# Performance work log

Hardware: AMD Instinct MI355X
Metric: run time of the kernel (lower is better)

Reference implementation:

```python
import jax, jax.numpy as jnp
import numpy as np
from jax import lax

# Module config (matches init_kwargs)
C_IN, C_OUT, D_STATE = 512, 256, 16
D_INNER = 2 * C_OUT          # canonical Mamba expand=2
DT_RANK = C_OUT // 16        # ceil(256/16) = 16
D_CONV = 4
BN_EPS = 1e-5


def setup_inputs() -> dict:
    key = jax.random.key(0)
    ks = jax.random.split(key, 16)
    s = 0.02
    B, H, W = 8, 64, 64
    inp = {
        "x": jax.random.normal(ks[0], (B, C_IN, H, W), jnp.float32),
        # lateral 1x1 conv
        "lateral_w": jax.random.normal(ks[1], (C_OUT, C_IN), jnp.float32) * s,
        "lateral_b": jnp.zeros((C_OUT,), jnp.float32),
        # mamba block params
        "in_proj_w": jax.random.normal(ks[2], (2 * D_INNER, C_OUT), jnp.float32) * s,
        "conv1d_w": jax.random.normal(ks[3], (D_INNER, D_CONV), jnp.float32) * s,
        "conv1d_b": jnp.zeros((D_INNER,), jnp.float32),
        "x_proj_w": jax.random.normal(ks[4], (DT_RANK + 2 * D_STATE, D_INNER), jnp.float32) * s,
        "dt_proj_w": jax.random.normal(ks[5], (D_INNER, DT_RANK), jnp.float32) * s,
        "dt_proj_b": jnp.full((D_INNER,), -4.0, jnp.float32),  # softplus -> small dt
        "A_log": jnp.log(jnp.broadcast_to(jnp.arange(1, D_STATE + 1, dtype=jnp.float32), (D_INNER, D_STATE))),  # S4D-real init
        "D_param": jnp.ones((D_INNER,), jnp.float32),
        "out_proj_w": jax.random.normal(ks[6], (C_OUT, D_INNER), jnp.float32) * s,
        # refine: 3x3 conv + BN (eval) + ReLU
        "refine_w": jax.random.normal(ks[7], (C_OUT, C_OUT, 3, 3), jnp.float32) * s,
        "refine_b": jnp.zeros((C_OUT,), jnp.float32),
        "bn_gamma": jnp.ones((C_OUT,), jnp.float32),
        "bn_beta": jnp.zeros((C_OUT,), jnp.float32),
        "bn_mean": jnp.zeros((C_OUT,), jnp.float32),
        "bn_var": jnp.ones((C_OUT,), jnp.float32),
    }
    return inp


def _silu(v):
    return v * jax.nn.sigmoid(v)


def _mamba(u, in_proj_w, conv1d_w, conv1d_b, x_proj_w, dt_proj_w, dt_proj_b,
           A_log, D_param, out_proj_w):
    """Canonical Mamba block on u: (B, L, D) -> (B, L, D)."""
    B, L, D = u.shape
    xz = jnp.einsum('bld,ed->ble', u, in_proj_w)            # (B,L,2*d_inner)
    xm, z = jnp.split(xz, 2, axis=-1)
    # causal depthwise conv1d over L
    xc = xm.transpose(0, 2, 1)                               # (B,d_inner,L)
    xc = lax.conv_general_dilated(xc, conv1d_w[:, None, :], (1,),
                                  [(D_CONV - 1, 0)],
                                  feature_group_count=D_INNER)
    xc = _silu(xc + conv1d_b[None, :, None]).transpose(0, 2, 1)  # (B,L,d_inner)
    proj = jnp.einsum('bld,ed->ble', xc, x_proj_w)           # (B,L,dt_rank+2*N)
    dt_r = proj[..., :DT_RANK]
    B_ssm = proj[..., DT_RANK:DT_RANK + D_STATE]             # (B,L,N)
    C_ssm = proj[..., DT_RANK + D_STATE:]                    # (B,L,N)
    dt = jax.nn.softplus(jnp.einsum('blr,dr->bld', dt_r, dt_proj_w) + dt_proj_b)
    A = -jnp.exp(A_log)                                      # (d_inner,N)

    def step(h, inputs):
        dt_t, B_t, C_t, x_t = inputs                         # (B,d), (B,N), (B,N), (B,d)
        dA = jnp.exp(dt_t[..., None] * A)                    # (B,d,N)
        h = dA * h + dt_t[..., None] * B_t[:, None, :] * x_t[..., None]
        y = jnp.einsum('bdn,bn->bd', h, C_t)
        return h, y

    xs = (dt.transpose(1, 0, 2), B_ssm.transpose(1, 0, 2),
          C_ssm.transpose(1, 0, 2), xc.transpose(1, 0, 2))
    h0 = jnp.zeros((B, D_INNER, D_STATE), u.dtype)
    _, ys = lax.scan(step, h0, xs)                           # (L,B,d_inner)
    y = ys.transpose(1, 0, 2) + xc * D_param
    y = y * _silu(z)
    return jnp.einsum('ble,de->bld', y, out_proj_w)          # (B,L,D)


def reference(x, lateral_w, lateral_b, in_proj_w, conv1d_w, conv1d_b, x_proj_w,
              dt_proj_w, dt_proj_b, A_log, D_param, out_proj_w, refine_w,
              refine_b, bn_gamma, bn_beta, bn_mean, bn_var):
    B, _, H, W = x.shape
    # lateral 1x1 conv
    xl = jnp.einsum('oi,bihw->bohw', lateral_w, x) + lateral_b[None, :, None, None]
    # mamba on flattened spatial sequence, residual add
    u = xl.reshape(B, C_OUT, H * W).transpose(0, 2, 1)        # (B,L,C)
    m = _mamba(u, in_proj_w, conv1d_w, conv1d_b, x_proj_w, dt_proj_w,
               dt_proj_b, A_log, D_param, out_proj_w)
    xr = xl + m.transpose(0, 2, 1).reshape(B, C_OUT, H, W)
    # refine: 3x3 conv + BN(eval) + ReLU
    r = lax.conv_general_dilated(xr, refine_w, (1, 1), [(1, 1), (1, 1)])
    r = r + refine_b[None, :, None, None]
    inv = bn_gamma / jnp.sqrt(bn_var + BN_EPS)
    r = (r - bn_mean[None, :, None, None]) * inv[None, :, None, None] + bn_beta[None, :, None, None]
    return jax.nn.relu(r)
```

## Files before the change

kernel.cpp:

```cpp
#include <hip/hip_runtime.h>
#include <math.h>

#define NB   8
#define CIN  512
#define COUT 256
#define DIN  512
#define LHW  4096
#define NCHK 256
#define CHL  16
#define PW   66
#define PPOS (PW*PW)

typedef __attribute__((ext_vector_type(8))) short bf16x8;
typedef __attribute__((ext_vector_type(4))) float f32x4;
typedef __attribute__((ext_vector_type(2))) float f32x2;

__device__ __forceinline__ float siluf(float v)  { return v / (1.f + __expf(-v)); }
__device__ __forceinline__ float splusf(float v) {
  return fmaxf(v, 0.f) + __logf(1.f + __expf(-fabsf(v)));
}

__device__ __forceinline__ unsigned short f2b(float f) {
  union { float f; unsigned u; } v; v.f = f;
  unsigned r = v.u + 0x7fff + ((v.u >> 16) & 1);
  return (unsigned short)(r >> 16);
}
__device__ __forceinline__ float b2f(unsigned int u) {
  union { unsigned u; float f; } v; v.u = (u & 0xffffu) << 16; return v.f;
}

__device__ __forceinline__ f32x2 pk_fma(f32x2 a, f32x2 b, f32x2 c) {
  f32x2 d;
  asm("v_pk_fma_f32 %0, %1, %2, %3" : "=v"(d) : "v"(a), "v"(b), "v"(c));
  return d;
}
__device__ __forceinline__ f32x2 pk_mul(f32x2 a, f32x2 b) {
  f32x2 d;
  asm("v_pk_mul_f32 %0, %1, %2" : "=v"(d) : "v"(a), "v"(b));
  return d;
}

__device__ __forceinline__ void gload16(const unsigned short* g, unsigned short* l) {
  __builtin_amdgcn_global_load_lds(
      (const __attribute__((address_space(1))) unsigned int*)g,
      (__attribute__((address_space(3))) unsigned int*)l, 16, 0, 0);
}

#define WO1 131072
#define WO2 393216
#define WO3 425984
#define WO4 557056
#define WO5 1146880
#define WO6 1474560
#define WPN 1482752
__global__ __launch_bounds__(256)
void k_wprep(const float* __restrict__ lw, const float* __restrict__ ipw,
             const float* __restrict__ xpw, const float* __restrict__ opw,
             const float* __restrict__ rw, const float* __restrict__ dtpw,
             const float* __restrict__ A_log,
             unsigned short* __restrict__ wb, unsigned short* __restrict__ wfb,
             float* __restrict__ Antab) {
  const int i = blockIdx.x * 256 + threadIdx.x;
  if (i < WO1)      wb[i] = f2b(lw[i]);
  else if (i < WO2) wb[i] = f2b(ipw[i - WO1]);
  else if (i < WO3) {
    const int j = i - WO2, row = j >> 9, col = j & 511;
    wb[i] = (row < 48) ? f2b(xpw[row * 512 + col]) : (unsigned short)0;
  }
  else if (i < WO4) wb[i] = f2b(opw[i - WO3]);
  else if (i < WO5) {
    const int j = i - WO4, o = j / 2304, kk = j % 2304;
    const int tap = kk >> 8, ch = kk & 255;
    wb[i] = f2b(rw[(o * 256 + ch) * 9 + tap]);
  }
  else if (i < WO6) {
    const int j = i - WO5, row = j >> 9, e = j & 511;
    float v = 0.f;
    if (row < 512) {
#pragma unroll
      for (int r = 0; r < 16; ++r)
        v = fmaf(dtpw[row * 16 + r], xpw[r * 512 + e], v);
    } else if (row < 560) {
      v = xpw[(row - 512) * 512 + e];
    }
    wfb[j] = f2b(v);
  }
  else if (i < WPN) {
    const int j = i - WO6;
    Antab[j] = -__expf(A_log[j]);
  }
}

__global__ __launch_bounds__(256)
void k_border(unsigned int* __restrict__ xrp_u) {
  const int i = blockIdx.x * 256 + threadIdx.x;
  if (i >= 8 * 260 * 128) return;
  const int b  = i / (260 * 128);
  const int r  = i - b * 260 * 128;
  const int p  = r >> 7;
  const int ci = r & 127;
  int y, x;
  if (p < 66)       { y = 0;       x = p; }
  else if (p < 132) { y = 65;      x = p - 66; }
  else if (p < 196) { x = 0;       y = p - 131; }
  else              { x = 65;      y = p - 195; }
  xrp_u[(((size_t)b * PPOS + y * PW + x) * COUT >> 1) + ci] = 0u;
}

__global__ __launch_bounds__(256)
void k_xpose(const float* __restrict__ x, unsigned short* __restrict__ xt) {
  __shared__ unsigned short Ts[64][80];
  const int b  = blockIdx.z;
  const int k0 = blockIdx.y * 64;
  const int l0 = blockIdx.x * 64;
  const int t  = threadIdx.x;
  const int tx = t & 15, ty = t >> 4;
#pragma unroll
  for (int r = 0; r < 4; ++r) {
    const int k = ty + r * 16;
    float4 v = *(const float4*)(x + ((size_t)b * CIN + k0 + k) * LHW + l0 + tx * 4);
    Ts[tx*4+0][k] = f2b(v.x);
    Ts[tx*4+1][k] = f2b(v.y);
    Ts[tx*4+2][k] = f2b(v.z);
    Ts[tx*4+3][k] = f2b(v.w);
  }
  __syncthreads();
  const int lr = t >> 2, kc = (t & 3) * 16;
  unsigned short* dst = xt + ((size_t)b * LHW + l0 + lr) * CIN + k0 + kc;
  *(uint4*)dst       = *(const uint4*)&Ts[lr][kc];
  *(uint4*)(dst + 8) = *(const uint4*)&Ts[lr][kc + 8];
}

template<int RSA, int RSB, int KTOT>
__device__ __forceinline__ void gemm_loop_128(
    const unsigned short* __restrict__ Ab, const unsigned short* __restrict__ Bb,
    unsigned short (&As)[2][4096], unsigned short (&Bs)[2][4096],
    int t, f32x4 acc[4][4]) {
  const int w = t >> 6, lane = t & 63;
  const int wm = w >> 1, wn = w & 1;
  const int arow = t >> 2;
  const int acol = (((t & 3) ^ ((t >> 3) & 3))) * 8;
  const int fr = lane & 15;
  const int g8 = ((lane >> 4) * 8) ^ (((fr >> 1) & 3) * 8);
  for (int k0 = 0; k0 < KTOT; k0 += 64) {
    __syncthreads();
    gload16(Ab + (size_t)arow * RSA + k0 + acol,             &As[0][w * 512]);
    gload16(Ab + (size_t)(64 + arow) * RSA + k0 + acol,      &As[0][2048 + w*512]);
    gload16(Bb + (size_t)arow * RSB + k0 + acol,             &Bs[0][w * 512]);
    gload16(Bb + (size_t)(64 + arow) * RSB + k0 + acol,      &Bs[0][2048 + w*512]);
    gload16(Ab + (size_t)arow * RSA + k0 + 32 + acol,        &As[1][w * 512]);
    gload16(Ab + (size_t)(64 + arow) * RSA + k0 + 32 + acol, &As[1][2048 + w*512]);
    gload16(Bb + (size_t)arow * RSB + k0 + 32 + acol,        &Bs[1][w * 512]);
    gload16(Bb + (size_t)(64 + arow) * RSB + k0 + 32 + acol, &Bs[1][2048 + w*512]);
    __syncthreads();
#pragma unroll
    for (int h = 0; h < 2; ++h) {
      bf16x8 af[4], bf[4];
#pragma unroll
      for (int f = 0; f < 4; ++f) {
        af[f] = *(const bf16x8*)&As[h][(wm*64 + f*16 + fr) * 32 + g8];
        bf[f] = *(const bf16x8*)&Bs[h][(wn*64 + f*16 + fr) * 32 + g8];
      }
#pragma unroll
      for (int i = 0; i < 4; ++i)
#pragma unroll
        for (int j = 0; j < 4; ++j)
          acc[i][j] = __builtin_amdgcn_mfma_f32_16x16x32_bf16(af[i], bf[j], acc[i][j], 0, 0, 0);
    }
  }
}

__global__ __launch_bounds__(256)
void k_lat_mfma(const unsigned short* __restrict__ xt, const unsigned short* __restrict__ lwb,
                const float* __restrict__ lb, unsigned short* __restrict__ ub) {
  __shared__ __align__(16) unsigned short As[2][4096], Bs[2][4096];
  const int t = threadIdx.x, lane = t & 63, w = t >> 6;
  const int wm = w >> 1, wn = w & 1;
  const int b = blockIdx.z, m0 = blockIdx.y * 128, n0 = blockIdx.x * 128;
  f32x4 acc[4][4] = {};
  gemm_loop_128<512, 512, 512>(xt + ((size_t)b * LHW + m0) * 512,
                               lwb + (size_t)n0 * 512, As, Bs, t, acc);
  const int fr = lane & 15, q4 = (lane >> 4) * 4;
#pragma unroll
  for (int i = 0; i < 4; ++i) {
    const int l = m0 + wm*64 + i*16 + q4;
#pragma unroll
    for (int j = 0; j < 4; ++j) {
      const int o = n0 + wn*64 + j*16 + fr;
      const float bias = lb[o];
      unsigned short* dst = ub + ((size_t)b * LHW + l) * COUT + o;
#pragma unroll
      for (int q = 0; q < 4; ++q)
        dst[(size_t)q * COUT] = f2b(acc[i][j][q] + bias);
    }
  }
}

__global__ __launch_bounds__(256)
void k_inproj_mfma(const unsigned short* __restrict__ ub, const unsigned short* __restrict__ ipwb,
                   unsigned short* __restrict__ xm_b, unsigned short* __restrict__ zsb) {
  __shared__ __align__(16) unsigned short As[2][4096], Bs[2][4096];
  const int t = threadIdx.x, lane = t & 63, w = t >> 6;
  const int wm = w >> 1, wn = w & 1;
  const int b = blockIdx.z, m0 = blockIdx.y * 128, n0 = blockIdx.x * 128;
  f32x4 acc[4][4] = {};
  gemm_loop_128<256, 256, 256>(ub + ((size_t)b * LHW + m0) * 256,
                               ipwb + (size_t)n0 * 256, As, Bs, t, acc);
  const int fr = lane & 15, q4 = (lane >> 4) * 4;
  const bool isz = (n0 >= 512);
#pragma unroll
  for (int i = 0; i < 4; ++i) {
    const int l = m0 + wm*64 + i*16 + q4;
#pragma unroll
    for (int j = 0; j < 4; ++j) {
      const int e = n0 + wn*64 + j*16 + fr;
      if (isz) {
        unsigned short* dst = zsb + ((size_t)b * LHW + l) * DIN + (e - 512);
#pragma unroll
        for (int q = 0; q < 4; ++q)
          dst[(size_t)q * DIN] = f2b(siluf(acc[i][j][q]));
      } else {
        unsigned short* dst = xm_b + ((size_t)b * LHW + l) * DIN + e;
#pragma unroll
        for (int q = 0; q < 4; ++q)
          dst[(size_t)q * DIN] = f2b(acc[i][j][q]);
      }
    }
  }
}

__global__ __launch_bounds__(256)
void k_conv1d(const unsigned short* __restrict__ xm_b, const float* __restrict__ cw,
              const float* __restrict__ cb, unsigned short* __restrict__ xc_b) {
  const int tid = blockIdx.x * 256 + threadIdx.x;
  const int e8 = tid & 63;
  const int lg = tid >> 6;
  const int l0 = (lg & 511) * 8;
  const int b  = lg >> 9;
  const int e0 = e8 * 8;
  float bias[8];
  *(float4*)&bias[0] = *(const float4*)(cb + e0);
  *(float4*)&bias[4] = *(const float4*)(cb + e0 + 4);
  float wv[8][4];
#pragma unroll
  for (int q = 0; q < 8; ++q) {
    float4 w4 = *(const float4*)(cw + (e0 + q) * 4);
    wv[q][0] = w4.x; wv[q][1] = w4.y; wv[q][2] = w4.z; wv[q][3] = w4.w;
  }
  const unsigned short* base = xm_b + ((size_t)b * LHW + l0) * DIN + e0;
  uint4 rows[11];
  const uint4 z4 = make_uint4(0u, 0u, 0u, 0u);
#pragma unroll
  for (int r = 0; r < 11; ++r) {
    const int ll = r - 3;
    rows[r] = (l0 + ll >= 0) ? *(const uint4*)(base + (ptrdiff_t)ll * DIN) : z4;
  }
  unsigned short* outb = xc_b + ((size_t)b * LHW + l0) * DIN + e0;
#pragma unroll
  for (int j = 0; j < 8; ++j) {
    float acc[8];
#pragma unroll
    for (int q = 0; q < 8; ++q) acc[q] = bias[q];
#pragma unroll
    for (int k = 0; k < 4; ++k) {
      const uint4 raw = rows[j + k];
      acc[0] = fmaf(b2f(raw.x),       wv[0][k], acc[0]);
      acc[1] = fmaf(b2f(raw.x >> 16), wv[1][k], acc[1]);
      acc[2] = fmaf(b2f(raw.y),       wv[2][k], acc[2]);
      acc[3] = fmaf(b2f(raw.y >> 16), wv[3][k], acc[3]);
      acc[4] = fmaf(b2f(raw.z),       wv[4][k], acc[4]);
      acc[5] = fmaf(b2f(raw.z >> 16), wv[5][k], acc[5]);
      acc[6] = fmaf(b2f(raw.w),       wv[6][k], acc[6]);
      acc[7] = fmaf(b2f(raw.w >> 16), wv[7][k], acc[7]);
    }
    uint4 o;
    o.x = (unsigned)f2b(siluf(acc[0])) | ((unsigned)f2b(siluf(acc[1])) << 16);
    o.y = (unsigned)f2b(siluf(acc[2])) | ((unsigned)f2b(siluf(acc[3])) << 16);
    o.z = (unsigned)f2b(siluf(acc[4])) | ((unsigned)f2b(siluf(acc[5])) << 16);
    o.w = (unsigned)f2b(siluf(acc[6])) | ((unsigned)f2b(siluf(acc[7])) << 16);
    *(uint4*)(outb + (size_t)j * DIN) = o;
  }
}

__global__ __launch_bounds__(256)
void k_xdt_mfma(const unsigned short* __restrict__ xc_b, const unsigned short* __restrict__ wfb,
                const float* __restrict__ dtpb,
                unsigned short* __restrict__ dtb, float* __restrict__ proj) {
  __shared__ __align__(16) unsigned short As[2][4096], Bs[2][4096];
  const int t = threadIdx.x, lane = t & 63, w = t >> 6;
  const int wm = w >> 1, wn = w & 1;
  const int b = blockIdx.z, m0 = blockIdx.x * 128, n0 = blockIdx.y * 128;
  f32x4 acc[4][4] = {};
  gemm_loop_128<512, 512, 512>(xc_b + ((size_t)b * LHW + m0) * 512,
                               wfb + (size_t)n0 * 512, As, Bs, t, acc);
  const int fr = lane & 15, q4 = (lane >> 4) * 4;
#pragma unroll
  for (int i = 0; i < 4; ++i) {
    const int l = m0 + wm*64 + i*16 + q4;
#pragma unroll
    for (int j = 0; j < 4; ++j) {
      const int c = n0 + wn*64 + j*16 + fr;
      if (c < 512) {
        const float bias = dtpb[c];
        unsigned short* dst = dtb + ((size_t)b * LHW + l) * 512 + c;
#pragma unroll
        for (int q = 0; q < 4; ++q)
          dst[(size_t)q * 512] = f2b(splusf(acc[i][j][q] + bias));
      } else if (c < 560) {
        float* dst = proj + ((size_t)b * LHW + l) * 48 + (c - 512);
#pragma unroll
        for (int q = 0; q < 4; ++q)
          dst[(size_t)q * 48] = acc[i][j][q];
      }
    }
  }
}

__global__ __launch_bounds__(512, 4)
void k_scanA(const float* __restrict__ proj, const unsigned short* __restrict__ dtb,
             const unsigned short* __restrict__ xc_b, const float* __restrict__ Antab,
             unsigned short* __restrict__ Sst, float* __restrict__ SDT) {
  __shared__ float prs[CHL * 16];
  const int bx = blockIdx.x;
  const int b = bx >> 8, c = bx & 255;
  const int d = threadIdx.x;
  const size_t rbase = (size_t)b * LHW + c * CHL;
  for (int i = d; i < CHL * 4; i += 512) {
    const int row = i >> 2, c4 = i & 3;
    *(float4*)&prs[row * 16 + c4 * 4] = *(const float4*)(proj + (rbase + row) * 48 + 16 + c4 * 4);
  }
  float An[16];
#pragma unroll
  for (int q = 0; q < 4; ++q)
    *(float4*)(&An[q*4]) = *(const float4*)(Antab + d*16 + q*4);
  f32x2 h2[8];
#pragma unroll
  for (int k = 0; k < 8; ++k) h2[k] = (f32x2){0.f, 0.f};
  const float An0 = An[0];
  bool lin = true;
#pragma unroll
  for (int n = 1; n < 16; ++n)
    lin = lin && (fabsf(An[n] - (n + 1) * An0) <= 1e-4f * fabsf(An[n]));
  float sdt = 0.f;
  const unsigned short* dt0 = dtb + rbase * 512 + d;
  const unsigned short* xc0 = xc_b + rbase * DIN + d;
  __syncthreads();
#pragma unroll
  for (int half = 0; half < CHL / 8; ++half) {
    float dtv[8], e1v[8];
#pragma unroll
    for (int u = 0; u < 8; ++u)
      dtv[u] = b2f(dt0[(size_t)(half * 8 + u) * 512]);
    if (lin) {
#pragma unroll
      for (int u = 0; u < 8; ++u)
        e1v[u] = __expf(dtv[u] * An0);
    }
#pragma unroll
    for (int u = 0; u < 8; ++u) {
      const int i = half * 8 + u;
      const float dt = dtv[u];
      sdt += dt;
      const float dtx = dt * b2f(xc0[(size_t)i * DIN]);
      const f32x2 dtx2 = (f32x2){dtx, dtx};
      f32x2 dA2[8];
      if (lin) {
        const float e1 = e1v[u];
        const float e2 = e1*e1, e3 = e2*e1, e4 = e2*e2, e8 = e4*e4;
        const f32x2 e4v = (f32x2){e4, e4}, e8v = (f32x2){e8, e8};
        dA2[0] = (f32x2){e1, e2};
        dA2[1] = (f32x2){e3, e4};
        dA2[2] = pk_mul(dA2[0], e4v);
        dA2[3] = pk_mul(dA2[1], e4v);
        dA2[4] = pk_mul(dA2[0], e8v);
        dA2[5] = pk_mul(dA2[1], e8v);
        dA2[6] = pk_mul(dA2[2], e8v);
        dA2[7] = pk_mul(dA2[3], e8v);
      } else {
#pragma unroll
        for (int k = 0; k < 8; ++k)
          dA2[k] = (f32x2){__expf(dt * An[2*k]), __expf(dt * An[2*k+1])};
      }
      const f32x2* B2 = (const f32x2*)&prs[i * 16];
#pragma unroll
      for (int k = 0; k < 8; ++k)
        h2[k] = pk_fma(dA2[k], h2[k], pk_mul(dtx2, B2[k]));
    }
  }
  unsigned short* o = Sst + ((size_t)bx * 512 + d) * 16;
  uint4 p0, p1;
  p0.x = (unsigned)f2b(h2[0].x) | ((unsigned)f2b(h2[0].y) << 16);
  p0.y = (unsigned)f2b(h2[1].x) | ((unsigned)f2b(h2[1].y) << 16);
  p0.z = (unsigned)f2b(h2[2].x) | ((unsigned)f2b(h2[2].y) << 16);
  p0.w = (unsigned)f2b(h2[3].x) | ((unsigned)f2b(h2[3].y) << 16);
  p1.x = (unsigned)f2b(h2[4].x) | ((unsigned)f2b(h2[4].y) << 16);
  p1.y = (unsigned)f2b(h2[5].x) | ((unsigned)f2b(h2[5].y) << 16);
  p1.z = (unsigned)f2b(h2[6].x) | ((unsigned)f2b(h2[6].y) << 16);
  p1.w = (unsigned)f2b(h2[7].x) | ((unsigned)f2b(h2[7].y) << 16);
  *(uint4*)o       = p0;
  *(uint4*)(o + 8) = p1;
  SDT[(size_t)bx * 512 + d] = sdt;
}

__global__ __launch_bounds__(256)
void k_scanB(const unsigned short* __restrict__ Sst, const float* __restrict__ SDT,
             const float* __restrict__ Antab, unsigned short* __restrict__ hst) {
  const int tid = blockIdx.x * 256 + threadIdx.x;
  const int n = tid & 15;
  const int d = (tid >> 4) & 511;
  const int b = tid >> 13;
  const float An = Antab[d * 16 + n];
  float h = 0.f;
  for (int c = 0; c < NCHK; ++c) {
    const size_t idx = (size_t)((b*NCHK + c)*512 + d);
    hst[idx*16 + n] = f2b(h);
    h = __expf(SDT[idx] * An) * h + b2f(Sst[idx*16 + n]);
  }
}

__global__ __launch_bounds__(512, 4)
void k_scanC(const float* __restrict__ proj, const unsigned short* __restrict__ dtb,
             const unsigned short* __restrict__ xc_b,
             const unsigned short* __restrict__ zsb, const unsigned short* __restrict__ hst,
             const float* __restrict__ Antab, const float* __restrict__ Dpar,
             unsigned short* __restrict__ ydata) {
  __shared__ float prs[CHL * 32];
  const int bx = blockIdx.x;
  const int b = bx >> 8, c = bx & 255;
  const int d = threadIdx.x;
  const size_t rbase = (size_t)b * LHW + c * CHL;
  for (int i = d; i < CHL * 8; i += 512) {
    const int row = i >> 3, c4 = i & 7;
    *(float4*)&prs[row * 32 + c4 * 4] = *(const float4*)(proj + (rbase + row) * 48 + 16 + c4 * 4);
  }
  float An[16];
#pragma unroll
  for (int q = 0; q < 4; ++q)
    *(float4*)(&An[q*4]) = *(const float4*)(Antab + d*16 + q*4);
  f32x2 h2[8];
  {
    const unsigned short* hsrc = hst + ((size_t)bx * 512 + d) * 16;
    uint4 p0 = *(const uint4*)hsrc;
    uint4 p1 = *(const uint4*)(hsrc + 8);
    h2[0] = (f32x2){b2f(p0.x), b2f(p0.x >> 16)};
    h2[1] = (f32x2){b2f(p0.y), b2f(p0.y >> 16)};
    h2[2] = (f32x2){b2f(p0.z), b2f(p0.z >> 16)};
    h2[3] = (f32x2){b2f(p0.w), b2f(p0.w >> 16)};
    h2[4] = (f32x2){b2f(p1.x), b2f(p1.x >> 16)};
    h2[5] = (f32x2){b2f(p1.y), b2f(p1.y >> 16)};
    h2[6] = (f32x2){b2f(p1.z), b2f(p1.z >> 16)};
    h2[7] = (f32x2){b2f(p1.w), b2f(p1.w >> 16)};
  }
  const float An0 = An[0];
  bool lin = true;
#pragma unroll
  for (int n = 1; n < 16; ++n)
    lin = lin && (fabsf(An[n] - (n + 1) * An0) <= 1e-4f * fabsf(An[n]));
  const float dp = Dpar[d];
  const unsigned short* dt0 = dtb + rbase * 512 + d;
  const unsigned short* xc0 = xc_b + rbase * DIN + d;
  const unsigned short* zs0 = zsb + rbase * DIN + d;
  unsigned short* y0 = ydata + rbase * DIN + d;
  __syncthreads();
#pragma unroll
  for (int half = 0; half < CHL / 8; ++half) {
    float dtv[8], e1v[8];
#pragma unroll
    for (int u = 0; u < 8; ++u)
      dtv[u] = b2f(dt0[(size_t)(half * 8 + u) * 512]);
    if (lin) {
#pragma unroll
      for (int u = 0; u < 8; ++u)
        e1v[u] = __expf(dtv[u] * An0);
    }
#pragma unroll
    for (int u = 0; u < 8; ++u) {
      const int i = half * 8 + u;
      const float dt = dtv[u];
      const float xt = b2f(xc0[(size_t)i * DIN]);
      const float zv = b2f(zs0[(size_t)i * DIN]);
      const float dtx = dt * xt;
      const f32x2 dtx2 = (f32x2){dtx, dtx};
      f32x2 dA2[8];
      if (lin) {
        const float e1 = e1v[u];
        const float e2 = e1*e1, e3 = e2*e1, e4 = e2*e2, e8 = e4*e4;
        const f32x2 e4v = (f32x2){e4, e4}, e8v = (f32x2){e8, e8};
        dA2[0] = (f32x2){e1, e2};
        dA2[1] = (f32x2){e3, e4};
        dA2[2] = pk_mul(dA2[0], e4v);
        dA2[3] = pk_mul(dA2[1], e4v);
        dA2[4] = pk_mul(dA2[0], e8v);
        dA2[5] = pk_mul(dA2[1], e8v);
        dA2[6] = pk_mul(dA2[2], e8v);
        dA2[7] = pk_mul(dA2[3], e8v);
      } else {
#pragma unroll
        for (int k = 0; k < 8; ++k)
          dA2[k] = (f32x2){__expf(dt * An[2*k]), __expf(dt * An[2*k+1])};
      }
      const f32x2* B2 = (const f32x2*)&prs[i * 32];
      const f32x2* C2 = (const f32x2*)&prs[i * 32 + 16];
      f32x2 ya = (f32x2){0.f, 0.f}, yb = (f32x2){0.f, 0.f};
#pragma unroll
      for (int k = 0; k < 8; ++k) {
        h2[k] = pk_fma(dA2[k], h2[k], pk_mul(dtx2, B2[k]));
        if (k & 1) yb = pk_fma(h2[k], C2[k], yb);
        else       ya = pk_fma(h2[k], C2[k], ya);
      }
      const float y = (ya.x + ya.y) + (yb.x + yb.y);
      const float ov = (y + xt * dp) * zv;
      y0[(size_t)i * DIN] = f2b(ov);
    }
  }
}

__global__ __launch_bounds__(256)
void k_outproj_mfma(const unsigned short* __restrict__ ydata, const unsigned short* __restrict__ opwb,
                    const unsigned short* __restrict__ ub, unsigned short* __restrict__ xrp) {
  __shared__ __align__(16) unsigned short As[2][4096], Bs[2][4096];
  const int t = threadIdx.x, lane = t & 63, w = t >> 6;
  const int wm = w >> 1, wn = w & 1;
  const int b = blockIdx.z, m0 = blockIdx.y * 128, n0 = blockIdx.x * 128;
  f32x4 acc[4][4] = {};
  gemm_loop_128<512, 512, 512>(ydata + ((size_t)b * LHW + m0) * 512,
                               opwb + (size_t)n0 * 512, As, Bs, t, acc);
  const int fr = lane & 15, q4 = (lane >> 4) * 4;
#pragma unroll
  for (int i = 0; i < 4; ++i) {
    const int lbase = m0 + wm*64 + i*16 + q4;
#pragma unroll
    for (int q = 0; q < 4; ++q) {
      const int l = lbase + q;
      const int pos = ((l >> 6) + 1) * PW + (l & 63) + 1;
#pragma unroll
      for (int j = 0; j < 4; ++j) {
        const int o = n0 + wn*64 + j*16 + fr;
        const float r = b2f(ub[((size_t)b * LHW + l) * COUT + o]);
        xrp[((size_t)b * PPOS + pos) * COUT + o] = f2b(acc[i][j][q] + r);
      }
    }
  }
}

__global__ __launch_bounds__(256)
void k_refine_mfma(const unsigned short* __restrict__ Aw,
                   const unsigned short* __restrict__ xrp,
                   const float* __restrict__ rb, const float* __restrict__ bng,
                   const float* __restrict__ bnb, const float* __restrict__ bnm,
                   const float* __restrict__ bnv, float* __restrict__ out) {
  __shared__ __align__(16) unsigned short As[4][4096], Bs[4][4096];
  const int t = threadIdx.x;
  const int lane = t & 63;
  const int w = t >> 6;
  const int wm = w >> 1, wn = w & 1;
  const int b  = blockIdx.z;
  const int m0 = blockIdx.y * 128;
  const int n0 = blockIdx.x * 128;
  const int y0 = n0 >> 6;
  const unsigned short* xb = xrp + (size_t)b * PPOS * COUT;
  const int arow = t >> 2;
  const int acol = (((t & 3) ^ ((t >> 3) & 3))) * 8;
  const int fr = lane & 15;
  const int g8 = ((lane >> 4) * 8) ^ (((fr >> 1) & 3) * 8);

#define RF_STAGE(ks, buf) {                                                            \
    const int tap_ = (ks) >> 3;                                                        \
    const int i0_  = ((ks) & 7) * 32;                                                  \
    const int ky_  = tap_ / 3, kx_ = tap_ - ky_ * 3;                                   \
    const int k0_  = tap_ * 256 + i0_;                                                 \
    const unsigned short* ga_ = Aw + (size_t)(m0 + arow) * 2304 + k0_ + acol;          \
    const unsigned short* gb_ = xb + ((size_t)((y0 + ky_) * PW + kx_ + arow)) * COUT + i0_ + acol; \
    gload16(ga_,              &As[buf][w * 512]);                                      \
    gload16(ga_ + 64 * 2304,  &As[buf][2048 + w * 512]);                               \
    gload16(gb_,              &Bs[buf][w * 512]);                                      \
    gload16(gb_ + PW * COUT,  &Bs[buf][2048 + w * 512]);                               \
  }

  f32x4 acc[4][4] = {};
  for (int ks = 0; ks < 72; ks += 4) {
    __syncthreads();
    RF_STAGE(ks, 0);
    RF_STAGE(ks + 1, 1);
    RF_STAGE(ks + 2, 2);
    RF_STAGE(ks + 3, 3);
    __syncthreads();
#pragma unroll
    for (int h = 0; h < 4; ++h) {
      bf16x8 af[4], bfr[4];
#pragma unroll
      for (int f = 0; f < 4; ++f) {
        af[f]  = *(const bf16x8*)&As[h][(wm*64 + f*16 + fr) * 32 + g8];
        bfr[f] = *(const bf16x8*)&Bs[h][(wn*64 + f*16 + fr) * 32 + g8];
      }
#pragma unroll
      for (int i = 0; i < 4; ++i)
#pragma unroll
        for (int j = 0; j < 4; ++j)
          acc[i][j] = __builtin_amdgcn_mfma_f32_16x16x32_bf16(af[i], bfr[j], acc[i][j], 0, 0, 0);
    }
  }
#undef RF_STAGE
  const int q4 = (lane >> 4) * 4;
#pragma unroll
  for (int i = 0; i < 4; ++i) {
    const int obase = m0 + wm*64 + i*16 + q4;
#pragma unroll
    for (int q = 0; q < 4; ++q) {
      const int o = obase + q;
      const float inv = bng[o] * rsqrtf(bnv[o] + 1e-5f);
      const float sh  = (rb[o] - bnm[o]) * inv + bnb[o];
      float* orow = out + ((size_t)b * COUT + o) * LHW + n0 + wn*64 + fr;
#pragma unroll
      for (int j = 0; j < 4; ++j)
        orow[j*16] = fmaxf(fmaf(acc[i][j][q], inv, sh), 0.f);
    }
  }
}

extern "C" void kernel_launch(void* const* d_in, const int* in_sizes, int n_in,
                              void* d_out, int out_size, void* d_ws, size_t ws_size,
                              hipStream_t stream) {
  const float* x    = (const float*)d_in[0];
  const float* lw   = (const float*)d_in[1];
  const float* lb   = (const float*)d_in[2];
  const float* ipw  = (const float*)d_in[3];
  const float* cw   = (const float*)d_in[4];
  const float* cb   = (const float*)d_in[5];
  const float* xpw  = (const float*)d_in[6];
  const float* dtpw = (const float*)d_in[7];
  const float* dtpb = (const float*)d_in[8];
  const float* Alog = (const float*)d_in[9];
  const float* Dpar = (const float*)d_in[10];
  const float* opw  = (const float*)d_in[11];
  const float* rw   = (const float*)d_in[12];
  const float* rb   = (const float*)d_in[13];
  const float* bng  = (const float*)d_in[14];
  const float* bnb  = (const float*)d_in[15];
  const float* bnm  = (const float*)d_in[16];
  const float* bnv  = (const float*)d_in[17];
  float* out = (float*)d_out;

  float* ws = (float*)d_ws;
  unsigned short* ub   = (unsigned short*)ws;
  unsigned short* xt   = (unsigned short*)(ws + 4194304);
  unsigned short* xm_b = (unsigned short*)(ws + 12582912);
  unsigned short* xc_b = (unsigned short*)(ws + 20971520);
  unsigned short* zsb  = (unsigned short*)(ws + 29360128);
  float* proj = ws + 37748736;
  unsigned short* Sst = (unsigned short*)(ws + 39321600);
  float* SDT  = ws + 47710208;
  unsigned short* hst = (unsigned short*)(ws + 48758784);
  unsigned short* wb  = (unsigned short*)(ws + 64487424);
  unsigned short* wfb = (unsigned short*)(ws + 65060864);
  float* Antab = ws + 65224704;
  unsigned short* lwb  = wb;
  unsigned short* ipwb = wb + WO1;
  unsigned short* opwb = wb + WO3;
  unsigned short* Aw   = wb + WO4;
  unsigned short* ydata = xm_b;
  unsigned short* dtb   = xt;
  unsigned short* xrp   = xt;

  k_wprep<<<dim3(5792), 256, 0, stream>>>(lw, ipw, xpw, opw, rw, dtpw, Alog, wb, wfb, Antab);
  k_xpose<<<dim3(64, 8, 8), 256, 0, stream>>>(x, xt);
  k_lat_mfma<<<dim3(2, 32, 8), 256, 0, stream>>>(xt, lwb, lb, ub);
  k_inproj_mfma<<<dim3(8, 32, 8), 256, 0, stream>>>(ub, ipwb, xm_b, zsb);
  k_conv1d<<<dim3(1024), 256, 0, stream>>>(xm_b, cw, cb, xc_b);
  k_xdt_mfma<<<dim3(32, 5, 8), 256, 0, stream>>>(xc_b, wfb, dtpb, dtb, proj);
  k_scanA<<<dim3(NB * NCHK), 512, 0, stream>>>(proj, dtb, xc_b, Antab, Sst, SDT);
  k_scanB<<<dim3(256), 256, 0, stream>>>(Sst, SDT, Antab, hst);
  k_scanC<<<dim3(NB * NCHK), 512, 0, stream>>>(proj, dtb, xc_b, zsb, hst, Antab, Dpar, ydata);
  k_border<<<dim3(1040), 256, 0, stream>>>((unsigned int*)xrp);
  k_outproj_mfma<<<dim3(2, 32, 8), 256, 0, stream>>>(ydata, opwb, ub, xrp);
  k_refine_mfma<<<dim3(32, 2, 8), 256, 0, stream>>>(Aw, xrp, rb, bng, bnb, bnm, bnv, out);
}
```

Before: 339.7 us.

## Split refine conv K dimension in two and combine with BN epilogue kernel

The 3x3 refine convolution GEMM is split into two K halves, which doubles the block count. Each half writes fp32 partial sums to workspace buffers. A new elementwise kernel sums the partials and applies bias, batch norm and ReLU. Shared memory staging drops from 4 to 2 stages per sync. This aims to raise occupancy and parallelism, at the cost of extra global traffic for the partial buffers and one more launch.

Result: slower. 361.8 us (+6.5%).

```diff
diff --git a/kernel.cpp b/kernel.cpp
--- a/kernel.cpp
+++ b/kernel.cpp
@@ -546,16 +546,15 @@
 __global__ __launch_bounds__(256)
 void k_refine_mfma(const unsigned short* __restrict__ Aw,
                    const unsigned short* __restrict__ xrp,
-                   const float* __restrict__ rb, const float* __restrict__ bng,
-                   const float* __restrict__ bnb, const float* __restrict__ bnm,
-                   const float* __restrict__ bnv, float* __restrict__ out) {
-  __shared__ __align__(16) unsigned short As[4][4096], Bs[4][4096];
+                   float* __restrict__ psum0, float* __restrict__ psum1) {
+  __shared__ __align__(16) unsigned short As[2][4096], Bs[2][4096];
   const int t = threadIdx.x;
   const int lane = t & 63;
   const int w = t >> 6;
   const int wm = w >> 1, wn = w & 1;
   const int b  = blockIdx.z;
-  const int m0 = blockIdx.y * 128;
+  const int m0 = (blockIdx.y & 1) * 128;
+  const int kh = blockIdx.y >> 1;
   const int n0 = blockIdx.x * 128;
   const int y0 = n0 >> 6;
   const unsigned short* xb = xrp + (size_t)b * PPOS * COUT;
@@ -578,15 +577,14 @@
   }
 
   f32x4 acc[4][4] = {};
-  for (int ks = 0; ks < 72; ks += 4) {
+  const int ks0 = kh * 36;
+  for (int ks = ks0; ks < ks0 + 36; ks += 2) {
     __syncthreads();
     RF_STAGE(ks, 0);
     RF_STAGE(ks + 1, 1);
-    RF_STAGE(ks + 2, 2);
-    RF_STAGE(ks + 3, 3);
     __syncthreads();
 #pragma unroll
-    for (int h = 0; h < 4; ++h) {
+    for (int h = 0; h < 2; ++h) {
       bf16x8 af[4], bfr[4];
 #pragma unroll
       for (int f = 0; f < 4; ++f) {
@@ -601,6 +599,7 @@
     }
   }
 #undef RF_STAGE
+  float* psum = kh ? psum1 : psum0;
   const int q4 = (lane >> 4) * 4;
 #pragma unroll
   for (int i = 0; i < 4; ++i) {
@@ -608,14 +607,32 @@
 #pragma unroll
     for (int q = 0; q < 4; ++q) {
       const int o = obase + q;
-      const float inv = bng[o] * rsqrtf(bnv[o] + 1e-5f);
-      const float sh  = (rb[o] - bnm[o]) * inv + bnb[o];
-      float* orow = out + ((size_t)b * COUT + o) * LHW + n0 + wn*64 + fr;
+      float* orow = psum + ((size_t)b * COUT + o) * LHW + n0 + wn*64 + fr;
 #pragma unroll
       for (int j = 0; j < 4; ++j)
-        orow[j*16] = fmaxf(fmaf(acc[i][j][q], inv, sh), 0.f);
-    }
-  }
+        orow[j*16] = acc[i][j][q];
+    }
+  }
+}
+
+__global__ __launch_bounds__(256)
+void k_bncomb(const float* __restrict__ psum0, const float* __restrict__ psum1,
+              const float* __restrict__ rb, const float* __restrict__ bng,
+              const float* __restrict__ bnb, const float* __restrict__ bnm,
+              const float* __restrict__ bnv, float* __restrict__ out) {
+  const int i = blockIdx.x * 256 + threadIdx.x;
+  const size_t idx4 = (size_t)i * 4;
+  const int o = (int)((idx4 >> 12) & 255);
+  const float inv = bng[o] * rsqrtf(bnv[o] + 1e-5f);
+  const float sh  = (rb[o] - bnm[o]) * inv + bnb[o];
+  float4 a = *(const float4*)(psum0 + idx4);
+  float4 c = *(const float4*)(psum1 + idx4);
+  float4 r;
+  r.x = fmaxf(fmaf(a.x + c.x, inv, sh), 0.f);
+  r.y = fmaxf(fmaf(a.y + c.y, inv, sh), 0.f);
+  r.z = fmaxf(fmaf(a.z + c.z, inv, sh), 0.f);
+  r.w = fmaxf(fmaf(a.w + c.w, inv, sh), 0.f);
+  *(float4*)(out + idx4) = r;
 }
 
 extern "C" void kernel_launch(void* const* d_in, const int* in_sizes, int n_in,
@@ -661,6 +678,8 @@
   unsigned short* ydata = xm_b;
   unsigned short* dtb   = xt;
   unsigned short* xrp   = xt;
+  float* psum0 = ws + 12582912;
+  float* psum1 = ws + 20971520;
 
   k_wprep<<<dim3(5792), 256, 0, stream>>>(lw, ipw, xpw, opw, rw, dtpw, Alog, wb, wfb, Antab);
   k_xpose<<<dim3(64, 8, 8), 256, 0, stream>>>(x, xt);
@@ -673,5 +692,6 @@
   k_scanC<<<dim3(NB * NCHK), 512, 0, stream>>>(proj, dtb, xc_b, zsb, hst, Antab, Dpar, ydata);
   k_border<<<dim3(1040), 256, 0, stream>>>((unsigned int*)xrp);
   k_outproj_mfma<<<dim3(2, 32, 8), 256, 0, stream>>>(ydata, opwb, ub, xrp);
-  k_refine_mfma<<<dim3(32, 2, 8), 256, 0, stream>>>(Aw, xrp, rb, bng, bnb, bnm, bnv, out);
-}
+  k_refine_mfma<<<dim3(32, 4, 8), 256, 0, stream>>>(Aw, xrp, psum0, psum1);
+  k_bncomb<<<dim3(8192), 256, 0, stream>>>(psum0, psum1, rb, bng, bnb, bnm, bnv, out);
+}
```
